# Kernel optimization log

Hardware: AMD Instinct MI355X
Metric: run time of the kernel (lower is better)

## Reference

```python
import jax, jax.numpy as jnp
import numpy as np
from jax import lax

THRESHOLD_ABS = 0.5
MIN_DISTANCE = 3
MAX_PEAKS = 65536  # fixed-size peak buffer (jit-compatible replacement for torch nonzero)


def setup_inputs() -> dict:
    key = jax.random.key(0)
    belive_map = jax.random.uniform(key, (8, 2, 1024, 1024), dtype=jnp.float32)
    return {"belive_map": belive_map}


def reference(belive_map):
    B, C, H, W = belive_map.shape
    k = 2 * MIN_DISTANCE + 1  # 7
    pad = k // 2
    # max_pool2d(kernel=7, stride=1, padding=3) == sliding-window max with -inf padding
    x_max = lax.reduce_window(
        belive_map, -jnp.inf, lax.max,
        window_dimensions=(1, 1, k, k),
        window_strides=(1, 1, 1, 1),
        padding=((0, 0), (0, 0), (pad, pad), (pad, pad)),
    )
    x_mask = x_max == belive_map
    # exclude_border: zero a band of width 2*min_distance on all four sides
    ex = 2 * MIN_DISTANCE
    x_mask = x_mask.at[..., :ex].set(False)
    x_mask = x_mask.at[..., -ex:].set(False)
    x_mask = x_mask.at[..., :ex, :].set(False)
    x_mask = x_mask.at[..., -ex:, :].set(False)
    x_mask = x_mask & (belive_map > THRESHOLD_ABS)

    mask_flat = x_mask.reshape(B, C * H * W)
    val_flat = belive_map.reshape(B, C * H * W)

    def pick(m, v):
        # fixed-size nonzero; padded entries get index -1
        idx = jnp.nonzero(m, size=MAX_PEAKS, fill_value=-1)[0]
        valid = idx >= 0
        safe = jnp.where(valid, idx, 0)
        scores = jnp.where(valid, v[safe], 0.0)
        c = safe // (H * W)
        rem = safe % (H * W)
        h = rem // W
        w = rem % W
        coords = jnp.stack([w, h], axis=-1)           # (x, y) == ind[:, [2, 1]]
        coords = jnp.where(valid[:, None], coords, -1)
        labels = jnp.where(valid, c + 1, 0)            # ind[:, 0] + 1
        return coords, labels, scores

    coordinates, labels, scores = jax.vmap(pick)(mask_flat, val_flat)
    # per-image (coordinates, labels, scores), batched with fixed MAX_PEAKS slots;
    # invalid slots: coords=-1, labels=0, scores=0
    return coordinates, labels, scores
```

## Files before the change

### kernel.cpp

```cpp
#include <hip/hip_runtime.h>

#define HW  (1024u*1024u)
#define CHW (2u*HW)
#define MAXP 65536u
#define LABEL_OFF 1048576u
#define SCORE_OFF 1572864u
#define NINF (-3.0e38f)
#define PAIRS_PER_CHUNK 512u

__device__ __forceinline__ float max3f(float a, float b, float c) {
    return fmaxf(fmaxf(a, b), c);
}

__device__ __forceinline__ unsigned mbcnt_lt(unsigned long long m) {
    unsigned lo = __builtin_amdgcn_mbcnt_lo((unsigned)m, 0u);
    return __builtin_amdgcn_mbcnt_hi((unsigned)(m >> 32), lo);
}

__global__ __launch_bounds__(256, 4) void mask_kernel(const float* __restrict__ map,
                                                      uint2* __restrict__ pairs,
                                                      unsigned* __restrict__ chunkCount) {
    __shared__ float4 rowbuf[2][2][258];
    __shared__ unsigned swscan[4];
    int bid0 = blockIdx.x;
    int bid = (bid0 & 7) * 128 + (bid0 >> 3);
    int tid = threadIdx.x;
    int stripe = bid & 63;
    int img = bid >> 6;
    int r0 = stripe << 4;
    int lane = tid & 63, wv = tid >> 6;
    const float4* __restrict__ base = (const float4*)(map + ((size_t)img << 20));
    const size_t pbase = (size_t)bid * PAIRS_PER_CHUNK;

    if (tid < 8) {
        float4 n4 = make_float4(NINF, NINF, NINF, NINF);
        rowbuf[(tid >> 2) & 1][(tid >> 1) & 1][(tid & 1) * 257] = n4;
    }

    int c0 = tid * 4;
    int cvm = 0;
    #pragma unroll
    for (int j = 0; j < 4; ++j) {
        int cc = c0 + j;
        if (cc >= 6 && cc <= 1017) cvm |= (1 << j);
    }

    float4 w[12];
    #pragma unroll
    for (int k = 0; k < 10; ++k) {
        int rr = r0 - 3 + k;
        w[k] = ((unsigned)rr < 1024u) ? base[rr * 256 + tid]
                                      : make_float4(NINF, NINF, NINF, NINF);
    }

    unsigned chunkOff = 0;

    #pragma unroll
    for (int p = 0; p < 8; ++p) {
        int rA = r0 + 2 * p;

        float4 s0 = w[(2 * p + 0) % 12], s1 = w[(2 * p + 1) % 12];
        float4 s2 = w[(2 * p + 2) % 12], s3 = w[(2 * p + 3) % 12];
        float4 s4 = w[(2 * p + 4) % 12], s5 = w[(2 * p + 5) % 12];
        float4 s6 = w[(2 * p + 6) % 12], s7 = w[(2 * p + 7) % 12];

        float4 c6, vmA, vmB;
        c6.x = fmaxf(max3f(s1.x, s2.x, s3.x), max3f(s4.x, s5.x, s6.x));
        c6.y = fmaxf(max3f(s1.y, s2.y, s3.y), max3f(s4.y, s5.y, s6.y));
        c6.z = fmaxf(max3f(s1.z, s2.z, s3.z), max3f(s4.z, s5.z, s6.z));
        c6.w = fmaxf(max3f(s1.w, s2.w, s3.w), max3f(s4.w, s5.w, s6.w));
        vmA.x = fmaxf(c6.x, s0.x); vmB.x = fmaxf(c6.x, s7.x);
        vmA.y = fmaxf(c6.y, s0.y); vmB.y = fmaxf(c6.y, s7.y);
        vmA.z = fmaxf(c6.z, s0.z); vmB.z = fmaxf(c6.z, s7.z);
        vmA.w = fmaxf(c6.w, s0.w); vmB.w = fmaxf(c6.w, s7.w);

        rowbuf[p & 1][0][tid + 1] = vmA;
        rowbuf[p & 1][1][tid + 1] = vmB;
        __syncthreads();

        if (p < 6) {
            int q1 = rA + 7, q2 = rA + 8;
            w[(2 * p + 10) % 12] = ((unsigned)q1 < 1024u) ? base[q1 * 256 + tid]
                                                          : make_float4(NINF, NINF, NINF, NINF);
            w[(2 * p + 11) % 12] = ((unsigned)q2 < 1024u) ? base[q2 * 256 + tid]
                                                          : make_float4(NINF, NINF, NINF, NINF);
        }

        float4 LA = rowbuf[p & 1][0][tid], RA = rowbuf[p & 1][0][tid + 2];
        float4 LB = rowbuf[p & 1][1][tid], RB = rowbuf[p & 1][1][tid + 2];

        float mA0 = max3f(max3f(LA.y, LA.z, LA.w),  max3f(vmA.x, vmA.y, vmA.z), vmA.w);
        float mA1 = max3f(max3f(LA.z, LA.w, vmA.x), max3f(vmA.y, vmA.z, vmA.w), RA.x);
        float mA2 = max3f(max3f(LA.w, vmA.x, vmA.y), max3f(vmA.z, vmA.w, RA.x), RA.y);
        float mA3 = max3f(max3f(vmA.x, vmA.y, vmA.z), max3f(vmA.w, RA.x, RA.y), RA.z);
        float mB0 = max3f(max3f(LB.y, LB.z, LB.w),  max3f(vmB.x, vmB.y, vmB.z), vmB.w);
        float mB1 = max3f(max3f(LB.z, LB.w, vmB.x), max3f(vmB.y, vmB.z, vmB.w), RB.x);
        float mB2 = max3f(max3f(LB.w, vmB.x, vmB.y), max3f(vmB.z, vmB.w, RB.x), RB.y);
        float mB3 = max3f(max3f(vmB.x, vmB.y, vmB.z), max3f(vmB.w, RB.x, RB.y), RB.z);

        float4 ctrA = s3, ctrB = s4;
        int fA0 = (ctrA.x == mA0) & (ctrA.x > 0.5f);
        int fA1 = (ctrA.y == mA1) & (ctrA.y > 0.5f);
        int fA2 = (ctrA.z == mA2) & (ctrA.z > 0.5f);
        int fA3 = (ctrA.w == mA3) & (ctrA.w > 0.5f);
        int fB0 = (ctrB.x == mB0) & (ctrB.x > 0.5f);
        int fB1 = (ctrB.y == mB1) & (ctrB.y > 0.5f);
        int fB2 = (ctrB.z == mB2) & (ctrB.z > 0.5f);
        int fB3 = (ctrB.w == mB3) & (ctrB.w > 0.5f);
        int nibA = (fA0 | (fA1 << 1) | (fA2 << 2) | (fA3 << 3)) & cvm;
        int nibB = (fB0 | (fB1 << 1) | (fB2 << 2) | (fB3 << 3)) & cvm;
        int rowokA = (rA >= 6) & (rA <= 1017);
        int rowokB = ((rA + 1) >= 6) & ((rA + 1) <= 1017);
        nibA = rowokA ? nibA : 0;
        nibB = rowokB ? nibB : 0;

        unsigned long long bA0 = __ballot(nibA & 1), bA1 = __ballot(nibA & 2);
        unsigned long long bA2 = __ballot(nibA & 4), bA3 = __ballot(nibA & 8);
        unsigned long long bB0 = __ballot(nibB & 1), bB1 = __ballot(nibB & 2);
        unsigned long long bB2 = __ballot(nibB & 4), bB3 = __ballot(nibB & 8);
        unsigned preT_A = mbcnt_lt(bA0) + mbcnt_lt(bA1) + mbcnt_lt(bA2) + mbcnt_lt(bA3);
        unsigned preT_B = mbcnt_lt(bB0) + mbcnt_lt(bB1) + mbcnt_lt(bB2) + mbcnt_lt(bB3);
        unsigned sumA = (unsigned)(__popcll(bA0) + __popcll(bA1) + __popcll(bA2) + __popcll(bA3));
        unsigned sumB = (unsigned)(__popcll(bB0) + __popcll(bB1) + __popcll(bB2) + __popcll(bB3));

        if (lane == 0) swscan[wv] = sumA | (sumB << 16);
        __syncthreads();
        unsigned preA = 0, preB = 0, sumAall = 0, sumBall = 0;
        #pragma unroll
        for (int k = 0; k < 4; ++k) {
            unsigned sv = swscan[k];
            if (k < wv) { preA += sv & 0xFFFFu; preB += sv >> 16; }
            sumAall += sv & 0xFFFFu; sumBall += sv >> 16;
        }
        unsigned posA = chunkOff + preA + preT_A;
        unsigned posB = chunkOff + sumAall + preB + preT_B;
        chunkOff += sumAall + sumBall;

        unsigned flatbase = ((unsigned)(img & 1) << 20) | ((unsigned)rA << 10)
                          | ((unsigned)tid * 4u);
        if (nibA & 1) pairs[pbase + posA++] = make_uint2(flatbase + 0u, __float_as_uint(ctrA.x));
        if (nibA & 2) pairs[pbase + posA++] = make_uint2(flatbase + 1u, __float_as_uint(ctrA.y));
        if (nibA & 4) pairs[pbase + posA++] = make_uint2(flatbase + 2u, __float_as_uint(ctrA.z));
        if (nibA & 8) pairs[pbase + posA++] = make_uint2(flatbase + 3u, __float_as_uint(ctrA.w));
        if (nibB & 1) pairs[pbase + posB++] = make_uint2(flatbase + 1024u, __float_as_uint(ctrB.x));
        if (nibB & 2) pairs[pbase + posB++] = make_uint2(flatbase + 1025u, __float_as_uint(ctrB.y));
        if (nibB & 4) pairs[pbase + posB++] = make_uint2(flatbase + 1026u, __float_as_uint(ctrB.z));
        if (nibB & 8) pairs[pbase + posB++] = make_uint2(flatbase + 1027u, __float_as_uint(ctrB.w));
    }

    if (tid == 0) chunkCount[bid] = chunkOff;
}

__global__ __launch_bounds__(1024) void scan_scatter(const uint2* __restrict__ pairs,
                                                     const unsigned* __restrict__ chunkCount,
                                                     float* __restrict__ out) {
    int g = blockIdx.x;
    int b = g >> 5;
    int cbase0 = (g & 31) * 4;
    int tid = threadIdx.x;
    int lane = tid & 63, wv = tid >> 6;

    __shared__ unsigned sBase[128];
    __shared__ unsigned sCnt[128];
    __shared__ unsigned sTot[2];

    if (tid < 128) {
        unsigned c = chunkCount[b * 128 + tid];
        sCnt[tid] = c;
        unsigned incl = c;
        #pragma unroll
        for (int off = 1; off < 64; off <<= 1) {
            unsigned nn = __shfl_up(incl, off, 64);
            if (lane >= off) incl += nn;
        }
        if (lane == 63) sTot[wv] = incl;
        sBase[tid] = incl - c;
    }
    __syncthreads();
    if (tid >= 64 && tid < 128) sBase[tid] += sTot[0];
    __syncthreads();
    unsigned total = sTot[0] + sTot[1];

    int half = tid >> 9;
    int idx  = tid & 511;
    #pragma unroll
    for (int k = 0; k < 2; ++k) {
        int cib = cbase0 + k * 2 + half;
        int blkC = b * 128 + cib;
        unsigned n = sCnt[cib];
        if (n > PAIRS_PER_CHUNK) n = PAIRS_PER_CHUNK;
        unsigned cb = sBase[cib];

        if ((unsigned)idx < n) {
            uint2 pr = pairs[(size_t)blkC * PAIRS_PER_CHUNK + idx];
            unsigned slot = cb + (unsigned)idx;
            if (slot < MAXP) {
                unsigned flat = pr.x;
                unsigned c = flat >> 20;
                unsigned h = (flat >> 10) & 1023u;
                unsigned wcol = flat & 1023u;
                unsigned o = b * MAXP + slot;
                float2 xy; xy.x = (float)wcol; xy.y = (float)h;
                ((float2*)out)[o]   = xy;
                out[LABEL_OFF + o]  = (float)(c + 1u);
                out[SCORE_OFF + o]  = __uint_as_float(pr.y);
            }
        }

        unsigned slot = ((unsigned)cib) * 512u + (unsigned)idx;
        if (slot >= total) {
            unsigned o = b * MAXP + slot;
            float2 neg1; neg1.x = -1.0f; neg1.y = -1.0f;
            ((float2*)out)[o]   = neg1;
            out[LABEL_OFF + o]  = 0.0f;
            out[SCORE_OFF + o]  = 0.0f;
        }
    }
}

extern "C" void kernel_launch(void* const* d_in, const int* in_sizes, int n_in,
                              void* d_out, int out_size, void* d_ws, size_t ws_size,
                              hipStream_t stream) {
    const float* map = (const float*)d_in[0];
    float* out = (float*)d_out;
    uint2* pairs = (uint2*)d_ws;
    unsigned* chunkCount = (unsigned*)((char*)d_ws + 4194304);

    mask_kernel<<<1024, 256, 0, stream>>>(map, pairs, chunkCount);
    scan_scatter<<<256, 1024, 0, stream>>>(pairs, chunkCount, out);
}
```

Measured before the change: 28.36 us.

## Software-pipeline cross-wave peak compaction to remove one barrier per row pair

Double-buffers the per-wave count scratch so each iteration's cross-wave prefix and scatter are deferred to the next iteration, after the barrier that already guards the row buffer. This drops the second __syncthreads per row pair, and the loop gets one extra tail iteration to flush the last pair. In exchange the previous iteration's flags, centers and prefix values are carried across iterations, which raises register pressure under the 4-blocks-per-SM launch bound.

```diff
diff --git a/kernel.cpp b/kernel.cpp
--- a/kernel.cpp
+++ b/kernel.cpp
@@ -21,7 +21,7 @@
                                                       uint2* __restrict__ pairs,
                                                       unsigned* __restrict__ chunkCount) {
     __shared__ float4 rowbuf[2][2][258];
-    __shared__ unsigned swscan[4];
+    __shared__ unsigned swscan[2][4];
     int bid0 = blockIdx.x;
     int bid = (bid0 & 7) * 128 + (bid0 >> 3);
     int tid = threadIdx.x;
@@ -55,27 +55,36 @@
 
     unsigned chunkOff = 0;
 
-    #pragma unroll
-    for (int p = 0; p < 8; ++p) {
+    int pnibA = 0, pnibB = 0;
+    float4 pctrA = make_float4(0, 0, 0, 0), pctrB = make_float4(0, 0, 0, 0);
+    unsigned pPreTA = 0, pPreTB = 0, pFlatbase = 0;
+
+    #pragma unroll
+    for (int p = 0; p <= 8; ++p) {
         int rA = r0 + 2 * p;
-
-        float4 s0 = w[(2 * p + 0) % 12], s1 = w[(2 * p + 1) % 12];
-        float4 s2 = w[(2 * p + 2) % 12], s3 = w[(2 * p + 3) % 12];
-        float4 s4 = w[(2 * p + 4) % 12], s5 = w[(2 * p + 5) % 12];
-        float4 s6 = w[(2 * p + 6) % 12], s7 = w[(2 * p + 7) % 12];
-
-        float4 c6, vmA, vmB;
-        c6.x = fmaxf(max3f(s1.x, s2.x, s3.x), max3f(s4.x, s5.x, s6.x));
-        c6.y = fmaxf(max3f(s1.y, s2.y, s3.y), max3f(s4.y, s5.y, s6.y));
-        c6.z = fmaxf(max3f(s1.z, s2.z, s3.z), max3f(s4.z, s5.z, s6.z));
-        c6.w = fmaxf(max3f(s1.w, s2.w, s3.w), max3f(s4.w, s5.w, s6.w));
-        vmA.x = fmaxf(c6.x, s0.x); vmB.x = fmaxf(c6.x, s7.x);
-        vmA.y = fmaxf(c6.y, s0.y); vmB.y = fmaxf(c6.y, s7.y);
-        vmA.z = fmaxf(c6.z, s0.z); vmB.z = fmaxf(c6.z, s7.z);
-        vmA.w = fmaxf(c6.w, s0.w); vmB.w = fmaxf(c6.w, s7.w);
-
-        rowbuf[p & 1][0][tid + 1] = vmA;
-        rowbuf[p & 1][1][tid + 1] = vmB;
+        float4 vmA, vmB, s3v, s4v;
+
+        if (p < 8) {
+            float4 s0 = w[(2 * p + 0) % 12], s1 = w[(2 * p + 1) % 12];
+            float4 s2 = w[(2 * p + 2) % 12], s3 = w[(2 * p + 3) % 12];
+            float4 s4 = w[(2 * p + 4) % 12], s5 = w[(2 * p + 5) % 12];
+            float4 s6 = w[(2 * p + 6) % 12], s7 = w[(2 * p + 7) % 12];
+
+            float4 c6;
+            c6.x = fmaxf(max3f(s1.x, s2.x, s3.x), max3f(s4.x, s5.x, s6.x));
+            c6.y = fmaxf(max3f(s1.y, s2.y, s3.y), max3f(s4.y, s5.y, s6.y));
+            c6.z = fmaxf(max3f(s1.z, s2.z, s3.z), max3f(s4.z, s5.z, s6.z));
+            c6.w = fmaxf(max3f(s1.w, s2.w, s3.w), max3f(s4.w, s5.w, s6.w));
+            vmA.x = fmaxf(c6.x, s0.x); vmB.x = fmaxf(c6.x, s7.x);
+            vmA.y = fmaxf(c6.y, s0.y); vmB.y = fmaxf(c6.y, s7.y);
+            vmA.z = fmaxf(c6.z, s0.z); vmB.z = fmaxf(c6.z, s7.z);
+            vmA.w = fmaxf(c6.w, s0.w); vmB.w = fmaxf(c6.w, s7.w);
+
+            rowbuf[p & 1][0][tid + 1] = vmA;
+            rowbuf[p & 1][1][tid + 1] = vmB;
+            s3v = s3; s4v = s4;
+        }
+
         __syncthreads();
 
         if (p < 6) {
@@ -86,66 +95,73 @@
                                                           : make_float4(NINF, NINF, NINF, NINF);
         }
 
-        float4 LA = rowbuf[p & 1][0][tid], RA = rowbuf[p & 1][0][tid + 2];
-        float4 LB = rowbuf[p & 1][1][tid], RB = rowbuf[p & 1][1][tid + 2];
-
-        float mA0 = max3f(max3f(LA.y, LA.z, LA.w),  max3f(vmA.x, vmA.y, vmA.z), vmA.w);
-        float mA1 = max3f(max3f(LA.z, LA.w, vmA.x), max3f(vmA.y, vmA.z, vmA.w), RA.x);
-        float mA2 = max3f(max3f(LA.w, vmA.x, vmA.y), max3f(vmA.z, vmA.w, RA.x), RA.y);
-        float mA3 = max3f(max3f(vmA.x, vmA.y, vmA.z), max3f(vmA.w, RA.x, RA.y), RA.z);
-        float mB0 = max3f(max3f(LB.y, LB.z, LB.w),  max3f(vmB.x, vmB.y, vmB.z), vmB.w);
-        float mB1 = max3f(max3f(LB.z, LB.w, vmB.x), max3f(vmB.y, vmB.z, vmB.w), RB.x);
-        float mB2 = max3f(max3f(LB.w, vmB.x, vmB.y), max3f(vmB.z, vmB.w, RB.x), RB.y);
-        float mB3 = max3f(max3f(vmB.x, vmB.y, vmB.z), max3f(vmB.w, RB.x, RB.y), RB.z);
-
-        float4 ctrA = s3, ctrB = s4;
-        int fA0 = (ctrA.x == mA0) & (ctrA.x > 0.5f);
-        int fA1 = (ctrA.y == mA1) & (ctrA.y > 0.5f);
-        int fA2 = (ctrA.z == mA2) & (ctrA.z > 0.5f);
-        int fA3 = (ctrA.w == mA3) & (ctrA.w > 0.5f);
-        int fB0 = (ctrB.x == mB0) & (ctrB.x > 0.5f);
-        int fB1 = (ctrB.y == mB1) & (ctrB.y > 0.5f);
-        int fB2 = (ctrB.z == mB2) & (ctrB.z > 0.5f);
-        int fB3 = (ctrB.w == mB3) & (ctrB.w > 0.5f);
-        int nibA = (fA0 | (fA1 << 1) | (fA2 << 2) | (fA3 << 3)) & cvm;
-        int nibB = (fB0 | (fB1 << 1) | (fB2 << 2) | (fB3 << 3)) & cvm;
-        int rowokA = (rA >= 6) & (rA <= 1017);
-        int rowokB = ((rA + 1) >= 6) & ((rA + 1) <= 1017);
-        nibA = rowokA ? nibA : 0;
-        nibB = rowokB ? nibB : 0;
-
-        unsigned long long bA0 = __ballot(nibA & 1), bA1 = __ballot(nibA & 2);
-        unsigned long long bA2 = __ballot(nibA & 4), bA3 = __ballot(nibA & 8);
-        unsigned long long bB0 = __ballot(nibB & 1), bB1 = __ballot(nibB & 2);
-        unsigned long long bB2 = __ballot(nibB & 4), bB3 = __ballot(nibB & 8);
-        unsigned preT_A = mbcnt_lt(bA0) + mbcnt_lt(bA1) + mbcnt_lt(bA2) + mbcnt_lt(bA3);
-        unsigned preT_B = mbcnt_lt(bB0) + mbcnt_lt(bB1) + mbcnt_lt(bB2) + mbcnt_lt(bB3);
-        unsigned sumA = (unsigned)(__popcll(bA0) + __popcll(bA1) + __popcll(bA2) + __popcll(bA3));
-        unsigned sumB = (unsigned)(__popcll(bB0) + __popcll(bB1) + __popcll(bB2) + __popcll(bB3));
-
-        if (lane == 0) swscan[wv] = sumA | (sumB << 16);
-        __syncthreads();
-        unsigned preA = 0, preB = 0, sumAall = 0, sumBall = 0;
-        #pragma unroll
-        for (int k = 0; k < 4; ++k) {
-            unsigned sv = swscan[k];
-            if (k < wv) { preA += sv & 0xFFFFu; preB += sv >> 16; }
-            sumAall += sv & 0xFFFFu; sumBall += sv >> 16;
-        }
-        unsigned posA = chunkOff + preA + preT_A;
-        unsigned posB = chunkOff + sumAall + preB + preT_B;
-        chunkOff += sumAall + sumBall;
-
-        unsigned flatbase = ((unsigned)(img & 1) << 20) | ((unsigned)rA << 10)
-                          | ((unsigned)tid * 4u);
-        if (nibA & 1) pairs[pbase + posA++] = make_uint2(flatbase + 0u, __float_as_uint(ctrA.x));
-        if (nibA & 2) pairs[pbase + posA++] = make_uint2(flatbase + 1u, __float_as_uint(ctrA.y));
-        if (nibA & 4) pairs[pbase + posA++] = make_uint2(flatbase + 2u, __float_as_uint(ctrA.z));
-        if (nibA & 8) pairs[pbase + posA++] = make_uint2(flatbase + 3u, __float_as_uint(ctrA.w));
-        if (nibB & 1) pairs[pbase + posB++] = make_uint2(flatbase + 1024u, __float_as_uint(ctrB.x));
-        if (nibB & 2) pairs[pbase + posB++] = make_uint2(flatbase + 1025u, __float_as_uint(ctrB.y));
-        if (nibB & 4) pairs[pbase + posB++] = make_uint2(flatbase + 1026u, __float_as_uint(ctrB.z));
-        if (nibB & 8) pairs[pbase + posB++] = make_uint2(flatbase + 1027u, __float_as_uint(ctrB.w));
+        if (p > 0) {
+            unsigned preA = 0, preB = 0, sumAall = 0, sumBall = 0;
+            #pragma unroll
+            for (int k = 0; k < 4; ++k) {
+                unsigned sv = swscan[(p - 1) & 1][k];
+                if (k < wv) { preA += sv & 0xFFFFu; preB += sv >> 16; }
+                sumAall += sv & 0xFFFFu; sumBall += sv >> 16;
+            }
+            unsigned posA = chunkOff + preA + pPreTA;
+            unsigned posB = chunkOff + sumAall + preB + pPreTB;
+            chunkOff += sumAall + sumBall;
+
+            if (pnibA & 1) pairs[pbase + posA++] = make_uint2(pFlatbase + 0u, __float_as_uint(pctrA.x));
+            if (pnibA & 2) pairs[pbase + posA++] = make_uint2(pFlatbase + 1u, __float_as_uint(pctrA.y));
+            if (pnibA & 4) pairs[pbase + posA++] = make_uint2(pFlatbase + 2u, __float_as_uint(pctrA.z));
+            if (pnibA & 8) pairs[pbase + posA++] = make_uint2(pFlatbase + 3u, __float_as_uint(pctrA.w));
+            if (pnibB & 1) pairs[pbase + posB++] = make_uint2(pFlatbase + 1024u, __float_as_uint(pctrB.x));
+            if (pnibB & 2) pairs[pbase + posB++] = make_uint2(pFlatbase + 1025u, __float_as_uint(pctrB.y));
+            if (pnibB & 4) pairs[pbase + posB++] = make_uint2(pFlatbase + 1026u, __float_as_uint(pctrB.z));
+            if (pnibB & 8) pairs[pbase + posB++] = make_uint2(pFlatbase + 1027u, __float_as_uint(pctrB.w));
+        }
+
+        if (p < 8) {
+            float4 LA = rowbuf[p & 1][0][tid], RA = rowbuf[p & 1][0][tid + 2];
+            float4 LB = rowbuf[p & 1][1][tid], RB = rowbuf[p & 1][1][tid + 2];
+
+            float mA0 = max3f(max3f(LA.y, LA.z, LA.w),  max3f(vmA.x, vmA.y, vmA.z), vmA.w);
+            float mA1 = max3f(max3f(LA.z, LA.w, vmA.x), max3f(vmA.y, vmA.z, vmA.w), RA.x);
+            float mA2 = max3f(max3f(LA.w, vmA.x, vmA.y), max3f(vmA.z, vmA.w, RA.x), RA.y);
+            float mA3 = max3f(max3f(vmA.x, vmA.y, vmA.z), max3f(vmA.w, RA.x, RA.y), RA.z);
+            float mB0 = max3f(max3f(LB.y, LB.z, LB.w),  max3f(vmB.x, vmB.y, vmB.z), vmB.w);
+            float mB1 = max3f(max3f(LB.z, LB.w, vmB.x), max3f(vmB.y, vmB.z, vmB.w), RB.x);
+            float mB2 = max3f(max3f(LB.w, vmB.x, vmB.y), max3f(vmB.z, vmB.w, RB.x), RB.y);
+            float mB3 = max3f(max3f(vmB.x, vmB.y, vmB.z), max3f(vmB.w, RB.x, RB.y), RB.z);
+
+            int fA0 = (s3v.x == mA0) & (s3v.x > 0.5f);
+            int fA1 = (s3v.y == mA1) & (s3v.y > 0.5f);
+            int fA2 = (s3v.z == mA2) & (s3v.z > 0.5f);
+            int fA3 = (s3v.w == mA3) & (s3v.w > 0.5f);
+            int fB0 = (s4v.x == mB0) & (s4v.x > 0.5f);
+            int fB1 = (s4v.y == mB1) & (s4v.y > 0.5f);
+            int fB2 = (s4v.z == mB2) & (s4v.z > 0.5f);
+            int fB3 = (s4v.w == mB3) & (s4v.w > 0.5f);
+            int nibA = (fA0 | (fA1 << 1) | (fA2 << 2) | (fA3 << 3)) & cvm;
+            int nibB = (fB0 | (fB1 << 1) | (fB2 << 2) | (fB3 << 3)) & cvm;
+            int rowokA = (rA >= 6) & (rA <= 1017);
+            int rowokB = ((rA + 1) >= 6) & ((rA + 1) <= 1017);
+            nibA = rowokA ? nibA : 0;
+            nibB = rowokB ? nibB : 0;
+
+            unsigned long long bA0 = __ballot(nibA & 1), bA1 = __ballot(nibA & 2);
+            unsigned long long bA2 = __ballot(nibA & 4), bA3 = __ballot(nibA & 8);
+            unsigned long long bB0 = __ballot(nibB & 1), bB1 = __ballot(nibB & 2);
+            unsigned long long bB2 = __ballot(nibB & 4), bB3 = __ballot(nibB & 8);
+            unsigned preT_A = mbcnt_lt(bA0) + mbcnt_lt(bA1) + mbcnt_lt(bA2) + mbcnt_lt(bA3);
+            unsigned preT_B = mbcnt_lt(bB0) + mbcnt_lt(bB1) + mbcnt_lt(bB2) + mbcnt_lt(bB3);
+            unsigned sumA = (unsigned)(__popcll(bA0) + __popcll(bA1) + __popcll(bA2) + __popcll(bA3));
+            unsigned sumB = (unsigned)(__popcll(bB0) + __popcll(bB1) + __popcll(bB2) + __popcll(bB3));
+
+            if (lane == 0) swscan[p & 1][wv] = sumA | (sumB << 16);
+
+            pnibA = nibA; pnibB = nibB;
+            pctrA = s3v;  pctrB = s4v;
+            pPreTA = preT_A; pPreTB = preT_B;
+            pFlatbase = ((unsigned)(img & 1) << 20) | ((unsigned)rA << 10)
+                      | ((unsigned)tid * 4u);
+        }
     }
 
     if (tid == 0) chunkCount[bid] = chunkOff;
```

Measured after the change: 28.83 us. No clear change (+1.7%).
